# Optimization experiments

Hardware: AMD Instinct MI355X
Metric: run time of the kernel (lower is better)

Reference implementation:

```python
import jax, jax.numpy as jnp
import numpy as np

N_NODES = 100000
N_EDGES = 1600000
MAX_RADIUS = 3.0
NUM_BASIS = 3
SQRT2 = 2.0 ** 0.5
# e3nn soft_one_hot_linspace 'smooth_finite' prefactor
C_SMOOTH = 1.14136 * float(np.exp(2.0))


def _sus(x):
    # smooth unit step: exp(-1/x) for x>0 else 0 (NaN-safe for grad)
    safe = jnp.where(x > 0.0, x, 1.0)
    return jnp.where(x > 0.0, jnp.exp(-1.0 / safe), 0.0)


def radial_embed(d):
    # soft_one_hot_linspace(d, 0, max_radius, 3, basis='smooth_finite', cutoff=True) * sqrt(num_basis)
    values = jnp.linspace(0.0, MAX_RADIUS, NUM_BASIS + 2)[1:-1]  # [3]
    step = MAX_RADIUS / (NUM_BASIS + 1)
    diff = (d[:, None] - values) / step  # [E,3]
    y = C_SMOOTH * _sus(diff + 1.0) * _sus(1.0 - diff)
    return y * (NUM_BASIS ** 0.5)


def fcnet(x, w1, w2):
    # e3nn FullyConnectedNet([3,16,numel], relu): normalized weights, normalize2mom(relu)=sqrt(2)*relu
    h = SQRT2 * jax.nn.relu(x @ (w1 / w1.shape[0] ** 0.5))
    return h @ (w2 / w2.shape[0] ** 0.5)


def reference(pos, feat, edge_src, edge_dst, fc1_w1, fc1_w2, core_w1, core_w2, fc3_w1, fc3_w2, conv_w, conv_b):
    n = pos.shape[0]
    z = edge_src.shape[0] / n  # average num neighbors
    edge_vec = pos[edge_dst] - pos[edge_src]
    d = jnp.sqrt(jnp.sum(edge_vec * edge_vec, axis=1))  # edges are self-loop-free -> d > 0
    emb = radial_embed(d)  # [E,3]

    # NOTE on e3nn math: with input/mid/output parities all even and sh = 0e+1o+2e,
    # the only parity-allowed paths producing nonzero output are the 0e (scalar) paths,
    # which contract against Y_0 = 1 ('component' normalization). The 4x1e block of the
    # mid irreps is identically zero (no parity-allowed path ever populates it), so the
    # math below (scalar block only, with e3nn path weights) is exactly equivalent.
    def conv(x, w1, w2, mul_in, mul_out, path_w):
        # per-edge weights from radial MLP; keep the 0e->0e instruction block
        w = fcnet(emb, w1, w2)[:, : mul_in * mul_out].reshape(-1, mul_in, mul_out)
        msg = path_w * jnp.einsum('euw,eu->ew', w, x[edge_src])
        return jax.ops.segment_sum(msg, edge_dst, num_segments=n) / z ** 0.5

    x = conv(feat, fc1_w1, fc1_w2, 3, 4, (1.0 / 3.0) ** 0.5)  # tp1: fan_in 3*1 -> pw=1/sqrt(3)
    for i in range(3):
        x = conv(x, core_w1[i], core_w2[i], 4, 4, 0.5)  # tp2 0e path: pw=sqrt(1/4)
    x = conv(x, fc3_w1, fc3_w2, 4, 16, 0.5)  # tp3: pw=sqrt(1/4)
    # Conv1d(16, 2, 1) == pointwise linear
    return x @ conv_w.T + conv_b


def setup_inputs():
    key = jax.random.key(0)
    ks = jax.random.split(key, 12)
    pos = jax.random.uniform(ks[0], (N_NODES, 3), dtype=jnp.float32)  # unit box -> all edge lengths < max_radius
    feat = jax.random.normal(ks[1], (N_NODES, 3), dtype=jnp.float32)
    edge_src = jax.random.randint(ks[2], (N_EDGES,), 0, N_NODES, dtype=jnp.int32)
    off = jax.random.randint(ks[3], (N_EDGES,), 1, N_NODES, dtype=jnp.int32)
    edge_dst = ((edge_src + off) % N_NODES).astype(jnp.int32)  # radius_graph has no self-loops
    return {
        'pos': pos,
        'feat': feat,
        'edge_src': edge_src,
        'edge_dst': edge_dst,
        'fc1_w1': jax.random.normal(ks[4], (3, 16), jnp.float32),
        'fc1_w2': jax.random.normal(ks[5], (16, 12), jnp.float32),
        'core_w1': jax.random.normal(ks[6], (3, 3, 16), jnp.float32),
        'core_w2': jax.random.normal(ks[7], (3, 16, 48), jnp.float32),
        'fc3_w1': jax.random.normal(ks[8], (3, 16), jnp.float32),
        'fc3_w2': jax.random.normal(ks[9], (16, 64), jnp.float32),
        'conv_w': jax.random.normal(ks[10], (2, 16), jnp.float32) * 0.25,
        'conv_b': jax.random.normal(ks[11], (2,), jnp.float32) * 0.1,
    }
```

## Files before the change

kernel.cpp:

```cpp
#include <hip/hip_runtime.h>


#define BCAP 4608
#define NBMAX 400

__device__ __forceinline__ float sus_f(float x) {
    return x > 0.0f ? __expf(-1.0f / x) : 0.0f;
}

__device__ __forceinline__ float uload(const float* p) {
    return __uint_as_float(__builtin_amdgcn_readfirstlane(__float_as_uint(*p)));
}

__global__ __launch_bounds__(1024) void k_bin(
    const int* __restrict__ src, const int* __restrict__ dst,
    int* __restrict__ gcur, int* __restrict__ ptmp,
    const float* __restrict__ fc3w2, const float* __restrict__ cw,
    float* __restrict__ gbuf,
    int nedges, int nb)
{
    __shared__ int cnt[NBMAX];
    __shared__ int gb[NBMAX];
    if (threadIdx.x < NBMAX) cnt[threadIdx.x] = 0;
    __syncthreads();

    int base = blockIdx.x * 8192 + threadIdx.x * 8;
    int pk[8]; int bk[8]; short r[8];
    int ss[8], dd[8];
    if (base + 7 < nedges) {
        int4 s0 = *(const int4*)&src[base];
        int4 s1 = *(const int4*)&src[base + 4];
        int4 d0 = *(const int4*)&dst[base];
        int4 d1 = *(const int4*)&dst[base + 4];
        ss[0]=s0.x; ss[1]=s0.y; ss[2]=s0.z; ss[3]=s0.w;
        ss[4]=s1.x; ss[5]=s1.y; ss[6]=s1.z; ss[7]=s1.w;
        dd[0]=d0.x; dd[1]=d0.y; dd[2]=d0.z; dd[3]=d0.w;
        dd[4]=d1.x; dd[5]=d1.y; dd[6]=d1.z; dd[7]=d1.w;
        #pragma unroll
        for (int i = 0; i < 8; ++i) {
            int b = dd[i] >> 8;
            bk[i] = b;
            pk[i] = (ss[i] << 8) | (dd[i] & 255);
            r[i] = (short)atomicAdd(&cnt[b], 1);
        }
    } else {
        #pragma unroll
        for (int i = 0; i < 8; ++i) {
            int e = base + i;
            if (e < nedges) {
                int s = src[e], t = dst[e];
                int b = t >> 8;
                bk[i] = b;
                pk[i] = (s << 8) | (t & 255);
                r[i] = (short)atomicAdd(&cnt[b], 1);
            } else bk[i] = -1;
        }
    }
    __syncthreads();
    if (threadIdx.x < NBMAX && threadIdx.x < nb) {
        int c = cnt[threadIdx.x];
        gb[threadIdx.x] = c > 0 ? atomicAdd(&gcur[threadIdx.x], c) : 0;
    }
    __syncthreads();
    #pragma unroll
    for (int i = 0; i < 8; ++i) {
        if (bk[i] >= 0) {
            int p = gb[bk[i]] + (int)r[i];
            if (p < BCAP)
                ptmp[bk[i] * BCAP + p] = pk[i];
        }
    }

    if (blockIdx.x == 0 && threadIdx.x < 128) {
        int idx = threadIdx.x;
        int k = idx >> 3, u = (idx >> 1) & 3, c = idx & 1;
        float s = 0.0f;
        #pragma unroll
        for (int w = 0; w < 16; ++w)
            s = fmaf(fc3w2[k * 64 + u * 16 + w], cw[c * 16 + w], s);
        gbuf[idx] = s;
    }
}

__global__ __launch_bounds__(1024) void k_build(
    const int* __restrict__ gcur, const int* __restrict__ ptmp,
    const float* __restrict__ pos,
    float4* __restrict__ ebuf, int2* __restrict__ offs2,
    int n, int nb)
{
    int b = blockIdx.x;
    int cnt = gcur[b]; if (cnt > BCAP) cnt = BCAP;
    int t = threadIdx.x;

    __shared__ int stage[BCAP];
    __shared__ int perm[BCAP];
    __shared__ int deg[256];
    __shared__ int loffs[256];
    __shared__ int cur[256];

    const int* tin = ptmp + b * BCAP;
    for (int j = t; j < cnt; j += 1024) stage[j] = tin[j];
    if (t < 256) deg[t] = 0;
    __syncthreads();

    for (int j = t; j < cnt; j += 1024)
        atomicAdd(&deg[stage[j] & 255], 1);
    __syncthreads();

    if (t < 64) {
        int d0 = deg[4 * t + 0], d1 = deg[4 * t + 1];
        int d2 = deg[4 * t + 2], d3 = deg[4 * t + 3];
        int s = d0 + d1 + d2 + d3;
        int x = s;
        #pragma unroll
        for (int off = 1; off < 64; off <<= 1) {
            int y = __shfl_up(x, off);
            if (t >= off) x += y;
        }
        int ex = x - s;
        int e0 = ex, e1 = ex + d0, e2 = e1 + d1, e3 = e2 + d2;
        loffs[4 * t + 0] = e0; cur[4 * t + 0] = e0;
        loffs[4 * t + 1] = e1; cur[4 * t + 1] = e1;
        loffs[4 * t + 2] = e2; cur[4 * t + 2] = e2;
        loffs[4 * t + 3] = e3; cur[4 * t + 3] = e3;
    }
    __syncthreads();

    int nid0 = b << 8;
    {
        int nn = n - nid0; if (nn > 256) nn = 256;
        if (t < nn) {
            int st = b * BCAP + loffs[t];
            offs2[nid0 + t] = make_int2(st, st + deg[t]);
        }
    }

    for (int j = t; j < cnt; j += 1024) {
        int pkd = stage[j];
        perm[atomicAdd(&cur[pkd & 255], 1)] = pkd;
    }
    __syncthreads();

    const float C = 1.14136f * 7.3890560989306495f;
    for (int j = t; j < cnt; j += 1024) {
        int pkd = perm[j];
        int s = pkd >> 8;
        int tt = nid0 | (pkd & 255);
        float dx = pos[3 * tt + 0] - pos[3 * s + 0];
        float dy = pos[3 * tt + 1] - pos[3 * s + 1];
        float dz = pos[3 * tt + 2] - pos[3 * s + 2];
        float d = sqrtf(dx * dx + dy * dy + dz * dz);
        float e0, e1, e2;
        { float f = (d - 0.75f) * (1.0f / 0.75f);
          e0 = C * sus_f(f + 1.0f) * sus_f(1.0f - f); }
        { float f = (d - 1.50f) * (1.0f / 0.75f);
          e1 = C * sus_f(f + 1.0f) * sus_f(1.0f - f); }
        { float f = (d - 2.25f) * (1.0f / 0.75f);
          e2 = C * sus_f(f + 1.0f) * sus_f(1.0f - f); }
        ebuf[(size_t)b * BCAP + j] = make_float4(__int_as_float(s), e0, e1, e2);
    }
}


__global__ __launch_bounds__(256) void k_node_l1(
    const float* __restrict__ feat, const float4* __restrict__ edata,
    const int2* __restrict__ offs2,
    const float* __restrict__ w1, const float* __restrict__ w2,
    float* __restrict__ xout, int n)
{
    __shared__ float lw[16 * 20];
    if (threadIdx.x < 192) {
        int k = threadIdx.x / 12, r = threadIdx.x % 12;
        lw[k * 20 + r] = w2[k * 12 + r];
    }
    __syncthreads();

    int g = blockIdx.x * 256 + threadIdx.x;
    int nd = g >> 2;
    if (nd >= n) return;
    int t = g & 3;

    float w1r[3][16];
    #pragma unroll
    for (int j = 0; j < 3; ++j)
        #pragma unroll
        for (int k = 0; k < 16; ++k) w1r[j][k] = uload(&w1[j * 16 + k]);

    float O[16][3];
    #pragma unroll
    for (int k = 0; k < 16; ++k)
        #pragma unroll
        for (int u = 0; u < 3; ++u) O[k][u] = 0.0f;

    int2 se = offs2[nd];
    for (int e = se.x + t; e < se.y; e += 4) {
        float4 ed = edata[e];
        int s = __float_as_int(ed.x);
        float f0 = feat[3 * s + 0], f1 = feat[3 * s + 1], f2 = feat[3 * s + 2];
        #pragma unroll
        for (int k = 0; k < 16; ++k) {
            float a = fmaf(ed.y, w1r[0][k], fmaf(ed.z, w1r[1][k], ed.w * w1r[2][k]));
            float h = a > 0.0f ? a : 0.0f;
            O[k][0] = fmaf(h, f0, O[k][0]);
            O[k][1] = fmaf(h, f1, O[k][1]);
            O[k][2] = fmaf(h, f2, O[k][2]);
        }
    }

    float p0 = 0.f, p1 = 0.f, p2 = 0.f, p3 = 0.f;
    #pragma unroll
    for (int k = 0; k < 16; ++k)
        #pragma unroll
        for (int u = 0; u < 3; ++u) {
            const float4 q = *(const float4*)&lw[k * 20 + u * 4];
            float o = O[k][u];
            p0 = fmaf(o, q.x, p0); p1 = fmaf(o, q.y, p1);
            p2 = fmaf(o, q.z, p2); p3 = fmaf(o, q.w, p3);
        }
    p0 += __shfl_xor(p0, 1); p1 += __shfl_xor(p1, 1);
    p2 += __shfl_xor(p2, 1); p3 += __shfl_xor(p3, 1);
    p0 += __shfl_xor(p0, 2); p1 += __shfl_xor(p1, 2);
    p2 += __shfl_xor(p2, 2); p3 += __shfl_xor(p3, 2);
    if (t == 0) {
        const float S = 0.051031036307982884f;
        float4 o; o.x = p0 * S; o.y = p1 * S; o.z = p2 * S; o.w = p3 * S;
        ((float4*)xout)[nd] = o;
    }
}

__global__ __launch_bounds__(256) void k_node_core(
    const float4* __restrict__ xin, const float4* __restrict__ edata,
    const int2* __restrict__ offs2,
    const float* __restrict__ w1, const float* __restrict__ w2,
    float* __restrict__ xout, int n)
{
    __shared__ float lw[16 * 20];
    {
        int idx = threadIdx.x;
        int k = idx >> 4, r = idx & 15;
        lw[k * 20 + r] = w2[k * 48 + r];
    }
    __syncthreads();

    int g = blockIdx.x * 256 + threadIdx.x;
    int nd = g >> 2;
    if (nd >= n) return;
    int t = g & 3;

    float w1r[3][16];
    #pragma unroll
    for (int j = 0; j < 3; ++j)
        #pragma unroll
        for (int k = 0; k < 16; ++k) w1r[j][k] = uload(&w1[j * 16 + k]);

    float O[16][4];
    #pragma unroll
    for (int k = 0; k < 16; ++k)
        #pragma unroll
        for (int u = 0; u < 4; ++u) O[k][u] = 0.0f;

    int2 se = offs2[nd];
    for (int e = se.x + t; e < se.y; e += 4) {
        float4 ed = edata[e];
        int s = __float_as_int(ed.x);
        float4 x = xin[s];
        #pragma unroll
        for (int k = 0; k < 16; ++k) {
            float a = fmaf(ed.y, w1r[0][k], fmaf(ed.z, w1r[1][k], ed.w * w1r[2][k]));
            float h = a > 0.0f ? a : 0.0f;
            O[k][0] = fmaf(h, x.x, O[k][0]);
            O[k][1] = fmaf(h, x.y, O[k][1]);
            O[k][2] = fmaf(h, x.z, O[k][2]);
            O[k][3] = fmaf(h, x.w, O[k][3]);
        }
    }

    float p0 = 0.f, p1 = 0.f, p2 = 0.f, p3 = 0.f;
    #pragma unroll
    for (int k = 0; k < 16; ++k)
        #pragma unroll
        for (int u = 0; u < 4; ++u) {
            const float4 q = *(const float4*)&lw[k * 20 + u * 4];
            float o = O[k][u];
            p0 = fmaf(o, q.x, p0); p1 = fmaf(o, q.y, p1);
            p2 = fmaf(o, q.z, p2); p3 = fmaf(o, q.w, p3);
        }
    p0 += __shfl_xor(p0, 1); p1 += __shfl_xor(p1, 1);
    p2 += __shfl_xor(p2, 1); p3 += __shfl_xor(p3, 1);
    p0 += __shfl_xor(p0, 2); p1 += __shfl_xor(p1, 2);
    p2 += __shfl_xor(p2, 2); p3 += __shfl_xor(p3, 2);
    if (t == 0) {
        const float S = 0.04419417382415922f;
        float4 o; o.x = p0 * S; o.y = p1 * S; o.z = p2 * S; o.w = p3 * S;
        ((float4*)xout)[nd] = o;
    }
}

__global__ __launch_bounds__(256) void k_node_fc3_final(
    const float4* __restrict__ xin, const float4* __restrict__ edata,
    const int2* __restrict__ offs2,
    const float* __restrict__ w1, const float* __restrict__ gbuf,
    const float* __restrict__ cb,
    float* __restrict__ out, int n)
{
    __shared__ float lg[128];
    if (threadIdx.x < 128) lg[threadIdx.x] = gbuf[threadIdx.x];
    __syncthreads();

    int g = blockIdx.x * 256 + threadIdx.x;
    int nd = g >> 2;
    if (nd >= n) return;
    int t = g & 3;

    float w1r[3][16];
    #pragma unroll
    for (int j = 0; j < 3; ++j)
        #pragma unroll
        for (int k = 0; k < 16; ++k) w1r[j][k] = uload(&w1[j * 16 + k]);

    float O[16][4];
    #pragma unroll
    for (int k = 0; k < 16; ++k)
        #pragma unroll
        for (int u = 0; u < 4; ++u) O[k][u] = 0.0f;

    int2 se = offs2[nd];
    for (int e = se.x + t; e < se.y; e += 4) {
        float4 ed = edata[e];
        int s = __float_as_int(ed.x);
        float4 x = xin[s];
        #pragma unroll
        for (int k = 0; k < 16; ++k) {
            float a = fmaf(ed.y, w1r[0][k], fmaf(ed.z, w1r[1][k], ed.w * w1r[2][k]));
            float h = a > 0.0f ? a : 0.0f;
            O[k][0] = fmaf(h, x.x, O[k][0]);
            O[k][1] = fmaf(h, x.y, O[k][1]);
            O[k][2] = fmaf(h, x.z, O[k][2]);
            O[k][3] = fmaf(h, x.w, O[k][3]);
        }
    }

    float a0 = 0.f, a1 = 0.f;
    #pragma unroll
    for (int k = 0; k < 16; ++k)
        #pragma unroll
        for (int u = 0; u < 4; ++u) {
            float o = O[k][u];
            const float2 q = *(const float2*)&lg[(k * 4 + u) * 2];
            a0 = fmaf(o, q.x, a0);
            a1 = fmaf(o, q.y, a1);
        }
    a0 += __shfl_xor(a0, 1); a1 += __shfl_xor(a1, 1);
    a0 += __shfl_xor(a0, 2); a1 += __shfl_xor(a1, 2);
    if (t == 0) {
        const float S = 0.04419417382415922f;
        float2 o; o.x = fmaf(a0, S, cb[0]); o.y = fmaf(a1, S, cb[1]);
        ((float2*)out)[nd] = o;
    }
}


extern "C" void kernel_launch(void* const* d_in, const int* in_sizes, int n_in,
                              void* d_out, int out_size, void* d_ws, size_t ws_size,
                              hipStream_t stream) {
    const float* pos     = (const float*)d_in[0];
    const float* feat    = (const float*)d_in[1];
    const int*   esrc    = (const int*)d_in[2];
    const int*   edst    = (const int*)d_in[3];
    const float* fc1_w1  = (const float*)d_in[4];
    const float* fc1_w2  = (const float*)d_in[5];
    const float* core_w1 = (const float*)d_in[6];
    const float* core_w2 = (const float*)d_in[7];
    const float* fc3_w1  = (const float*)d_in[8];
    const float* fc3_w2  = (const float*)d_in[9];
    const float* conv_w  = (const float*)d_in[10];
    const float* conv_b  = (const float*)d_in[11];
    float* out = (float*)d_out;

    const int E = in_sizes[2];
    const int N = in_sizes[0] / 3;
    const int nb = (N + 255) >> 8;

    float4* ebuf = (float4*)d_ws;
    int* ptmp  = (int*)(ebuf + (size_t)nb * BCAP);
    float* xa  = (float*)(ptmp + (size_t)nb * BCAP);
    float* xb  = xa + (size_t)4 * N;
    int2* offs2 = (int2*)(xb + (size_t)4 * N);
    int* gcur  = (int*)(offs2 + N);
    float* gbuf = (float*)(gcur + ((nb + 3) & ~3));

    int g4 = (4 * N + 255) / 256;

    hipMemsetAsync(gcur, 0, (size_t)nb * sizeof(int), stream);
    k_bin<<<(E + 8191) / 8192, 1024, 0, stream>>>(esrc, edst, gcur, ptmp,
                                                  fc3_w2, conv_w, gbuf, E, nb);
    k_build<<<nb, 1024, 0, stream>>>(gcur, ptmp, pos, ebuf, offs2, N, nb);

    k_node_l1<<<g4, 256, 0, stream>>>(feat, ebuf, offs2, fc1_w1, fc1_w2, xa, N);
    k_node_core<<<g4, 256, 0, stream>>>((const float4*)xa, ebuf, offs2,
                                        core_w1 + 0, core_w2 + 0, xb, N);
    k_node_core<<<g4, 256, 0, stream>>>((const float4*)xb, ebuf, offs2,
                                        core_w1 + 48, core_w2 + 768, xa, N);
    k_node_core<<<g4, 256, 0, stream>>>((const float4*)xa, ebuf, offs2,
                                        core_w1 + 96, core_w2 + 1536, xb, N);
    k_node_fc3_final<<<g4, 256, 0, stream>>>((const float4*)xb, ebuf, offs2,
                                             fc3_w1, gbuf, conv_b, out, N);
}
```

Before: 215.9 us.

## Map hidden units to lanes: 16 threads per node each owning one hidden unit

```diff
diff --git a/kernel.cpp b/kernel.cpp
--- a/kernel.cpp
+++ b/kernel.cpp
@@ -6,10 +6,6 @@
 
 __device__ __forceinline__ float sus_f(float x) {
     return x > 0.0f ? __expf(-1.0f / x) : 0.0f;
-}
-
-__device__ __forceinline__ float uload(const float* p) {
-    return __uint_as_float(__builtin_amdgcn_readfirstlane(__float_as_uint(*p)));
 }
 
 __global__ __launch_bounds__(1024) void k_bin(
@@ -168,62 +164,45 @@
     const float* __restrict__ w1, const float* __restrict__ w2,
     float* __restrict__ xout, int n)
 {
-    __shared__ float lw[16 * 20];
-    if (threadIdx.x < 192) {
-        int k = threadIdx.x / 12, r = threadIdx.x % 12;
-        lw[k * 20 + r] = w2[k * 12 + r];
-    }
-    __syncthreads();
-
-    int g = blockIdx.x * 256 + threadIdx.x;
-    int nd = g >> 2;
+    int tid = threadIdx.x;
+    int k = tid & 15;
+    int nd = blockIdx.x * 16 + (tid >> 4);
     if (nd >= n) return;
-    int t = g & 3;
-
-    float w1r[3][16];
-    #pragma unroll
-    for (int j = 0; j < 3; ++j)
-        #pragma unroll
-        for (int k = 0; k < 16; ++k) w1r[j][k] = uload(&w1[j * 16 + k]);
-
-    float O[16][3];
-    #pragma unroll
-    for (int k = 0; k < 16; ++k)
-        #pragma unroll
-        for (int u = 0; u < 3; ++u) O[k][u] = 0.0f;
-
+
+    float w10 = w1[k], w11 = w1[16 + k], w12 = w1[32 + k];
+    float W[12];
+    #pragma unroll
+    for (int u = 0; u < 3; ++u) {
+        float4 q = *(const float4*)&w2[k * 12 + u * 4];
+        W[u * 4 + 0] = q.x; W[u * 4 + 1] = q.y;
+        W[u * 4 + 2] = q.z; W[u * 4 + 3] = q.w;
+    }
+
+    float O0 = 0.f, O1 = 0.f, O2 = 0.f;
     int2 se = offs2[nd];
-    for (int e = se.x + t; e < se.y; e += 4) {
+    #pragma unroll 4
+    for (int e = se.x; e < se.y; ++e) {
         float4 ed = edata[e];
         int s = __float_as_int(ed.x);
-        float f0 = feat[3 * s + 0], f1 = feat[3 * s + 1], f2 = feat[3 * s + 2];
-        #pragma unroll
-        for (int k = 0; k < 16; ++k) {
-            float a = fmaf(ed.y, w1r[0][k], fmaf(ed.z, w1r[1][k], ed.w * w1r[2][k]));
-            float h = a > 0.0f ? a : 0.0f;
-            O[k][0] = fmaf(h, f0, O[k][0]);
-            O[k][1] = fmaf(h, f1, O[k][1]);
-            O[k][2] = fmaf(h, f2, O[k][2]);
-        }
-    }
-
-    float p0 = 0.f, p1 = 0.f, p2 = 0.f, p3 = 0.f;
-    #pragma unroll
-    for (int k = 0; k < 16; ++k)
-        #pragma unroll
-        for (int u = 0; u < 3; ++u) {
-            const float4 q = *(const float4*)&lw[k * 20 + u * 4];
-            float o = O[k][u];
-            p0 = fmaf(o, q.x, p0); p1 = fmaf(o, q.y, p1);
-            p2 = fmaf(o, q.z, p2); p3 = fmaf(o, q.w, p3);
-        }
-    p0 += __shfl_xor(p0, 1); p1 += __shfl_xor(p1, 1);
-    p2 += __shfl_xor(p2, 1); p3 += __shfl_xor(p3, 1);
-    p0 += __shfl_xor(p0, 2); p1 += __shfl_xor(p1, 2);
-    p2 += __shfl_xor(p2, 2); p3 += __shfl_xor(p3, 2);
-    if (t == 0) {
+        float a = fmaf(ed.y, w10, fmaf(ed.z, w11, ed.w * w12));
+        float h = a > 0.0f ? a : 0.0f;
+        O0 = fmaf(h, feat[3 * s + 0], O0);
+        O1 = fmaf(h, feat[3 * s + 1], O1);
+        O2 = fmaf(h, feat[3 * s + 2], O2);
+    }
+
+    float t0 = fmaf(O0, W[0], fmaf(O1, W[4], O2 * W[8]));
+    float t1 = fmaf(O0, W[1], fmaf(O1, W[5], O2 * W[9]));
+    float t2 = fmaf(O0, W[2], fmaf(O1, W[6], O2 * W[10]));
+    float t3 = fmaf(O0, W[3], fmaf(O1, W[7], O2 * W[11]));
+    #pragma unroll
+    for (int off = 1; off < 16; off <<= 1) {
+        t0 += __shfl_xor(t0, off); t1 += __shfl_xor(t1, off);
+        t2 += __shfl_xor(t2, off); t3 += __shfl_xor(t3, off);
+    }
+    if (k == 0) {
         const float S = 0.051031036307982884f;
-        float4 o; o.x = p0 * S; o.y = p1 * S; o.z = p2 * S; o.w = p3 * S;
+        float4 o; o.x = t0 * S; o.y = t1 * S; o.z = t2 * S; o.w = t3 * S;
         ((float4*)xout)[nd] = o;
     }
 }
@@ -234,64 +213,47 @@
     const float* __restrict__ w1, const float* __restrict__ w2,
     float* __restrict__ xout, int n)
 {
-    __shared__ float lw[16 * 20];
-    {
-        int idx = threadIdx.x;
-        int k = idx >> 4, r = idx & 15;
-        lw[k * 20 + r] = w2[k * 48 + r];
-    }
-    __syncthreads();
-
-    int g = blockIdx.x * 256 + threadIdx.x;
-    int nd = g >> 2;
+    int tid = threadIdx.x;
+    int k = tid & 15;
+    int nd = blockIdx.x * 16 + (tid >> 4);
     if (nd >= n) return;
-    int t = g & 3;
-
-    float w1r[3][16];
-    #pragma unroll
-    for (int j = 0; j < 3; ++j)
-        #pragma unroll
-        for (int k = 0; k < 16; ++k) w1r[j][k] = uload(&w1[j * 16 + k]);
-
-    float O[16][4];
-    #pragma unroll
-    for (int k = 0; k < 16; ++k)
-        #pragma unroll
-        for (int u = 0; u < 4; ++u) O[k][u] = 0.0f;
-
+
+    float w10 = w1[k], w11 = w1[16 + k], w12 = w1[32 + k];
+    float W[16];
+    #pragma unroll
+    for (int u = 0; u < 4; ++u) {
+        float4 q = *(const float4*)&w2[k * 48 + u * 4];
+        W[u * 4 + 0] = q.x; W[u * 4 + 1] = q.y;
+        W[u * 4 + 2] = q.z; W[u * 4 + 3] = q.w;
+    }
+
+    float O0 = 0.f, O1 = 0.f, O2 = 0.f, O3 = 0.f;
     int2 se = offs2[nd];
-    for (int e = se.x + t; e < se.y; e += 4) {
+    #pragma unroll 4
+    for (int e = se.x; e < se.y; ++e) {
         float4 ed = edata[e];
         int s = __float_as_int(ed.x);
         float4 x = xin[s];
-        #pragma unroll
-        for (int k = 0; k < 16; ++k) {
-            float a = fmaf(ed.y, w1r[0][k], fmaf(ed.z, w1r[1][k], ed.w * w1r[2][k]));
-            float h = a > 0.0f ? a : 0.0f;
-            O[k][0] = fmaf(h, x.x, O[k][0]);
-            O[k][1] = fmaf(h, x.y, O[k][1]);
-            O[k][2] = fmaf(h, x.z, O[k][2]);
-            O[k][3] = fmaf(h, x.w, O[k][3]);
-        }
-    }
-
-    float p0 = 0.f, p1 = 0.f, p2 = 0.f, p3 = 0.f;
-    #pragma unroll
-    for (int k = 0; k < 16; ++k)
-        #pragma unroll
-        for (int u = 0; u < 4; ++u) {
-            const float4 q = *(const float4*)&lw[k * 20 + u * 4];
-            float o = O[k][u];
-            p0 = fmaf(o, q.x, p0); p1 = fmaf(o, q.y, p1);
-            p2 = fmaf(o, q.z, p2); p3 = fmaf(o, q.w, p3);
-        }
-    p0 += __shfl_xor(p0, 1); p1 += __shfl_xor(p1, 1);
-    p2 += __shfl_xor(p2, 1); p3 += __shfl_xor(p3, 1);
-    p0 += __shfl_xor(p0, 2); p1 += __shfl_xor(p1, 2);
-    p2 += __shfl_xor(p2, 2); p3 += __shfl_xor(p3, 2);
-    if (t == 0) {
+        float a = fmaf(ed.y, w10, fmaf(ed.z, w11, ed.w * w12));
+        float h = a > 0.0f ? a : 0.0f;
+        O0 = fmaf(h, x.x, O0);
+        O1 = fmaf(h, x.y, O1);
+        O2 = fmaf(h, x.z, O2);
+        O3 = fmaf(h, x.w, O3);
+    }
+
+    float t0 = fmaf(O0, W[0], fmaf(O1, W[4], fmaf(O2, W[8],  O3 * W[12])));
+    float t1 = fmaf(O0, W[1], fmaf(O1, W[5], fmaf(O2, W[9],  O3 * W[13])));
+    float t2 = fmaf(O0, W[2], fmaf(O1, W[6], fmaf(O2, W[10], O3 * W[14])));
+    float t3 = fmaf(O0, W[3], fmaf(O1, W[7], fmaf(O2, W[11], O3 * W[15])));
+    #pragma unroll
+    for (int off = 1; off < 16; off <<= 1) {
+        t0 += __shfl_xor(t0, off); t1 += __shfl_xor(t1, off);
+        t2 += __shfl_xor(t2, off); t3 += __shfl_xor(t3, off);
+    }
+    if (k == 0) {
         const float S = 0.04419417382415922f;
-        float4 o; o.x = p0 * S; o.y = p1 * S; o.z = p2 * S; o.w = p3 * S;
+        float4 o; o.x = t0 * S; o.y = t1 * S; o.z = t2 * S; o.w = t3 * S;
         ((float4*)xout)[nd] = o;
     }
 }
@@ -303,58 +265,44 @@
     const float* __restrict__ cb,
     float* __restrict__ out, int n)
 {
-    __shared__ float lg[128];
-    if (threadIdx.x < 128) lg[threadIdx.x] = gbuf[threadIdx.x];
-    __syncthreads();
-
-    int g = blockIdx.x * 256 + threadIdx.x;
-    int nd = g >> 2;
+    int tid = threadIdx.x;
+    int k = tid & 15;
+    int nd = blockIdx.x * 16 + (tid >> 4);
     if (nd >= n) return;
-    int t = g & 3;
-
-    float w1r[3][16];
-    #pragma unroll
-    for (int j = 0; j < 3; ++j)
-        #pragma unroll
-        for (int k = 0; k < 16; ++k) w1r[j][k] = uload(&w1[j * 16 + k]);
-
-    float O[16][4];
-    #pragma unroll
-    for (int k = 0; k < 16; ++k)
-        #pragma unroll
-        for (int u = 0; u < 4; ++u) O[k][u] = 0.0f;
-
+
+    float w10 = w1[k], w11 = w1[16 + k], w12 = w1[32 + k];
+    float G[8];
+    {
+        float4 q0 = *(const float4*)&gbuf[k * 8];
+        float4 q1 = *(const float4*)&gbuf[k * 8 + 4];
+        G[0] = q0.x; G[1] = q0.y; G[2] = q0.z; G[3] = q0.w;
+        G[4] = q1.x; G[5] = q1.y; G[6] = q1.z; G[7] = q1.w;
+    }
+
+    float O0 = 0.f, O1 = 0.f, O2 = 0.f, O3 = 0.f;
     int2 se = offs2[nd];
-    for (int e = se.x + t; e < se.y; e += 4) {
+    #pragma unroll 4
+    for (int e = se.x; e < se.y; ++e) {
         float4 ed = edata[e];
         int s = __float_as_int(ed.x);
         float4 x = xin[s];
-        #pragma unroll
-        for (int k = 0; k < 16; ++k) {
-            float a = fmaf(ed.y, w1r[0][k], fmaf(ed.z, w1r[1][k], ed.w * w1r[2][k]));
-            float h = a > 0.0f ? a : 0.0f;
-            O[k][0] = fmaf(h, x.x, O[k][0]);
-            O[k][1] = fmaf(h, x.y, O[k][1]);
-            O[k][2] = fmaf(h, x.z, O[k][2]);
-            O[k][3] = fmaf(h, x.w, O[k][3]);
-        }
-    }
-
-    float a0 = 0.f, a1 = 0.f;
-    #pragma unroll
-    for (int k = 0; k < 16; ++k)
-        #pragma unroll
-        for (int u = 0; u < 4; ++u) {
-            float o = O[k][u];
-            const float2 q = *(const float2*)&lg[(k * 4 + u) * 2];
-            a0 = fmaf(o, q.x, a0);
-            a1 = fmaf(o, q.y, a1);
-        }
-    a0 += __shfl_xor(a0, 1); a1 += __shfl_xor(a1, 1);
-    a0 += __shfl_xor(a0, 2); a1 += __shfl_xor(a1, 2);
-    if (t == 0) {
+        float a = fmaf(ed.y, w10, fmaf(ed.z, w11, ed.w * w12));
+        float h = a > 0.0f ? a : 0.0f;
+        O0 = fmaf(h, x.x, O0);
+        O1 = fmaf(h, x.y, O1);
+        O2 = fmaf(h, x.z, O2);
+        O3 = fmaf(h, x.w, O3);
+    }
+
+    float t0 = fmaf(O0, G[0], fmaf(O1, G[2], fmaf(O2, G[4], O3 * G[6])));
+    float t1 = fmaf(O0, G[1], fmaf(O1, G[3], fmaf(O2, G[5], O3 * G[7])));
+    #pragma unroll
+    for (int off = 1; off < 16; off <<= 1) {
+        t0 += __shfl_xor(t0, off); t1 += __shfl_xor(t1, off);
+    }
+    if (k == 0) {
         const float S = 0.04419417382415922f;
-        float2 o; o.x = fmaf(a0, S, cb[0]); o.y = fmaf(a1, S, cb[1]);
+        float2 o; o.x = fmaf(t0, S, cb[0]); o.y = fmaf(t1, S, cb[1]);
         ((float2*)out)[nd] = o;
     }
 }
@@ -389,20 +337,20 @@
     int* gcur  = (int*)(offs2 + N);
     float* gbuf = (float*)(gcur + ((nb + 3) & ~3));
 
-    int g4 = (4 * N + 255) / 256;
+    int g16 = (N + 15) / 16;
 
     hipMemsetAsync(gcur, 0, (size_t)nb * sizeof(int), stream);
     k_bin<<<(E + 8191) / 8192, 1024, 0, stream>>>(esrc, edst, gcur, ptmp,
                                                   fc3_w2, conv_w, gbuf, E, nb);
     k_build<<<nb, 1024, 0, stream>>>(gcur, ptmp, pos, ebuf, offs2, N, nb);
 
-    k_node_l1<<<g4, 256, 0, stream>>>(feat, ebuf, offs2, fc1_w1, fc1_w2, xa, N);
-    k_node_core<<<g4, 256, 0, stream>>>((const float4*)xa, ebuf, offs2,
-                                        core_w1 + 0, core_w2 + 0, xb, N);
-    k_node_core<<<g4, 256, 0, stream>>>((const float4*)xb, ebuf, offs2,
-                                        core_w1 + 48, core_w2 + 768, xa, N);
-    k_node_core<<<g4, 256, 0, stream>>>((const float4*)xa, ebuf, offs2,
-                                        core_w1 + 96, core_w2 + 1536, xb, N);
-    k_node_fc3_final<<<g4, 256, 0, stream>>>((const float4*)xb, ebuf, offs2,
-                                             fc3_w1, gbuf, conv_b, out, N);
-}
+    k_node_l1<<<g16, 256, 0, stream>>>(feat, ebuf, offs2, fc1_w1, fc1_w2, xa, N);
+    k_node_core<<<g16, 256, 0, stream>>>((const float4*)xa, ebuf, offs2,
+                                         core_w1 + 0, core_w2 + 0, xb, N);
+    k_node_core<<<g16, 256, 0, stream>>>((const float4*)xb, ebuf, offs2,
+                                         core_w1 + 48, core_w2 + 768, xa, N);
+    k_node_core<<<g16, 256, 0, stream>>>((const float4*)xa, ebuf, offs2,
+                                         core_w1 + 96, core_w2 + 1536, xb, N);
+    k_node_fc3_final<<<g16, 256, 0, stream>>>((const float4*)xb, ebuf, offs2,
+                                              fc3_w1, gbuf, conv_b, out, N);
+}
```

New measurement: 308.1 us. +42.7%, slower.
